# Performance work log

Measured on AMD Instinct MI355X. Metric: run time of the kernel, lower is better.

Reference implementation:

```python
import jax, jax.numpy as jnp
import numpy as np


def setup_inputs() -> dict:
    key = jax.random.key(0)
    ks = jax.random.split(key, 8)
    B, L, D, N, DM = 2, 2048, 2048, 8, 1024
    return {
        "x": jax.random.normal(ks[0], (B, L, D), jnp.float32),
        "A_log": jax.random.normal(ks[1], (D, N), jnp.float32),
        "x_proj_w": jax.random.normal(ks[2], (2 * N, D), jnp.float32) * (D ** -0.5),
        "x_proj_b": jax.random.normal(ks[3], (2 * N,), jnp.float32) * 0.02,
        "dt_proj_w": jax.random.normal(ks[4], (D, D), jnp.float32) * (D ** -0.5),
        "dt_proj_b": jax.random.normal(ks[5], (D,), jnp.float32) * 0.02,
        "out_proj_w": jax.random.normal(ks[6], (DM, D), jnp.float32) * (D ** -0.5),
        "out_proj_b": jax.random.normal(ks[7], (DM,), jnp.float32) * 0.02,
    }


def reference(x, A_log, x_proj_w, x_proj_b, dt_proj_w, dt_proj_b, out_proj_w, out_proj_b):
    # x: (B, L, D);  A_log: (D, N)
    A = -jnp.exp(A_log)                                   # (D, N), negative -> stable decay
    x_dbl = x @ x_proj_w.T + x_proj_b                     # (B, L, 2N): per-token B_t, C_t
    Bm, Cm = jnp.split(x_dbl, 2, axis=-1)                 # each (B, L, N)
    dt = jax.nn.softplus(x @ dt_proj_w.T + dt_proj_b)     # (B, L, D) selective timestep

    Bsz, L, D = x.shape
    N = A_log.shape[1]

    def step(h, inp):
        dt_t, B_t, C_t, x_t = inp                         # (B,D),(B,N),(B,N),(B,D)
        dA = jnp.exp(dt_t[..., None] * A)                 # (B, D, N)
        dB = dt_t[..., None] * B_t[:, None, :]            # (B, D, N)
        h = dA * h + dB * x_t[..., None]                  # (B, D, N)
        y = jnp.einsum("bdn,bn->bd", h, C_t)              # (B, D)
        return h, y

    h0 = jnp.zeros((Bsz, D, N), x.dtype)
    xs = (dt.transpose(1, 0, 2), Bm.transpose(1, 0, 2),
          Cm.transpose(1, 0, 2), x.transpose(1, 0, 2))
    _, ys = jax.lax.scan(step, h0, xs)                    # ys: (L, B, D)
    y = ys.transpose(1, 0, 2)                             # (B, L, D)
    return y @ out_proj_w.T + out_proj_b                  # (B, L, d_model)
```

## Files before the change

kernel.cpp:

```cpp
#include <hip/hip_runtime.h>
#include <hip/hip_bf16.h>

constexpr int Bsz = 2;
constexpr int L   = 2048;
constexpr int D   = 2048;
constexpr int Nst = 8;
constexpr int DM  = 1024;
constexpr int M   = Bsz * L;

constexpr int CH  = 64;
constexpr int T   = L / CH;
constexpr int BDN = Bsz * D * Nst;

typedef __bf16 bf16x8 __attribute__((ext_vector_type(8)));
typedef float f32x4 __attribute__((ext_vector_type(4)));

__global__ void cvt_f32_bf16(const float* __restrict__ in, __bf16* __restrict__ out, int n4) {
    int i = blockIdx.x * blockDim.x + threadIdx.x;
    if (i >= n4) return;
    float4 v = reinterpret_cast<const float4*>(in)[i];
    union { __bf16 b[4]; ushort4 u; } cv;
    cv.b[0] = (__bf16)v.x; cv.b[1] = (__bf16)v.y; cv.b[2] = (__bf16)v.z; cv.b[3] = (__bf16)v.w;
    reinterpret_cast<ushort4*>(out)[i] = cv.u;
}

__global__ __launch_bounds__(256) void xdbl_kernel(
    const float* __restrict__ x, const float* __restrict__ w,
    const float* __restrict__ bias, float* __restrict__ xdbl)
{
    const int lane = threadIdx.x & 63;
    const int row  = (blockIdx.x * blockDim.x + threadIdx.x) >> 6;
    if (row >= M) return;
    const float* xr = x + (size_t)row * D;
    float acc[16];
#pragma unroll
    for (int j = 0; j < 16; ++j) acc[j] = 0.f;
    for (int k = lane * 4; k < D; k += 64 * 4) {
        float4 xv = *reinterpret_cast<const float4*>(&xr[k]);
#pragma unroll
        for (int j = 0; j < 16; ++j) {
            float4 wv = *reinterpret_cast<const float4*>(&w[j * D + k]);
            acc[j] += xv.x * wv.x + xv.y * wv.y + xv.z * wv.z + xv.w * wv.w;
        }
    }
#pragma unroll
    for (int j = 0; j < 16; ++j) {
        float v = acc[j];
#pragma unroll
        for (int off = 32; off > 0; off >>= 1) v += __shfl_down(v, off, 64);
        if (lane == 0) xdbl[(size_t)row * 16 + j] = v + bias[j];
    }
}

__device__ inline void async16(__bf16* lds, const __bf16* g) {
    __builtin_amdgcn_global_load_lds(
        (const __attribute__((address_space(1))) void*)g,
        (__attribute__((address_space(3))) void*)lds, 16, 0, 0);
}

template <int MODE>
__global__ __launch_bounds__(256) void gemm_bt(
    const __bf16* __restrict__ A, const __bf16* __restrict__ Bw,
    const float* __restrict__ bias, float* __restrict__ C,
    int N, int K)
{
    constexpr int BM = 128, BN = 128, BK = 32;
    __shared__ __attribute__((aligned(16))) __bf16 lA[BM * BK];
    __shared__ __attribute__((aligned(16))) __bf16 lB[BN * BK];

    const int tid  = threadIdx.x;
    const int lane = tid & 63;
    const int wid  = tid >> 6;
    const int wm   = wid >> 1, wn = wid & 1;
    const int rowBase = blockIdx.y * BM;
    const int colBase = blockIdx.x * BN;
    const int lrow = lane & 15;
    const int kgrp = lane >> 4;

    f32x4 acc[4][4];
#pragma unroll
    for (int i = 0; i < 4; ++i)
#pragma unroll
        for (int j = 0; j < 4; ++j) acc[i][j] = f32x4{0.f, 0.f, 0.f, 0.f};

    const int sr = tid >> 2;
    const int sc = (tid & 3) * 8;
    const __bf16* gA0 = A  + (size_t)(rowBase + sr)      * K + sc;
    const __bf16* gA1 = A  + (size_t)(rowBase + sr + 64) * K + sc;
    const __bf16* gB0 = Bw + (size_t)(colBase + sr)      * K + sc;
    const __bf16* gB1 = Bw + (size_t)(colBase + sr + 64) * K + sc;
    __bf16* lA0p = &lA[tid * 8];
    __bf16* lA1p = &lA[2048 + tid * 8];
    __bf16* lB0p = &lB[tid * 8];
    __bf16* lB1p = &lB[2048 + tid * 8];

    for (int k0 = 0; k0 < K; k0 += BK) {
        async16(lA0p, gA0 + k0);
        async16(lA1p, gA1 + k0);
        async16(lB0p, gB0 + k0);
        async16(lB1p, gB1 + k0);
        __syncthreads();

        bf16x8 af[4], bfr[4];
#pragma unroll
        for (int m = 0; m < 4; ++m)
            af[m] = *reinterpret_cast<const bf16x8*>(&lA[(wm * 64 + m * 16 + lrow) * BK + kgrp * 8]);
#pragma unroll
        for (int n = 0; n < 4; ++n)
            bfr[n] = *reinterpret_cast<const bf16x8*>(&lB[(wn * 64 + n * 16 + lrow) * BK + kgrp * 8]);
#pragma unroll
        for (int m = 0; m < 4; ++m)
#pragma unroll
            for (int n = 0; n < 4; ++n)
                acc[m][n] = __builtin_amdgcn_mfma_f32_16x16x32_bf16(af[m], bfr[n], acc[m][n], 0, 0, 0);
        __syncthreads();
    }

#pragma unroll
    for (int m = 0; m < 4; ++m) {
        const int row = rowBase + wm * 64 + m * 16 + kgrp * 4;
#pragma unroll
        for (int n = 0; n < 4; ++n) {
            const int col = colBase + wn * 64 + n * 16 + lrow;
            const float bv = bias[col];
#pragma unroll
            for (int r = 0; r < 4; ++r) {
                float v = acc[m][n][r] + bv;
                if (MODE == 1) v = (v > 20.f) ? v : log1pf(expf(v));
                C[(size_t)(row + r) * N + col] = v;
            }
        }
    }
}

__global__ __launch_bounds__(64) void scan_p1(
    const float* __restrict__ dt, const float* __restrict__ x,
    const float* __restrict__ xdbl, const float* __restrict__ A_log,
    float* __restrict__ P, float* __restrict__ Hloc)
{
    const int tid = threadIdx.x;
    int blk = blockIdx.x;
    const int c  = blk % CH;  blk /= CH;
    const int dg = blk % (D / 64);
    const int b  = blk / (D / 64);
    const int d  = dg * 64 + tid;

    float A[Nst], h[Nst], p[Nst];
#pragma unroll
    for (int n = 0; n < Nst; ++n) {
        A[n] = -expf(A_log[(size_t)d * Nst + n]);
        h[n] = 0.f; p[n] = 1.f;
    }

    __shared__ __attribute__((aligned(16))) float sBC[T * 16];
    const float4* src = reinterpret_cast<const float4*>(xdbl + ((size_t)b * L + c * T) * 16);
#pragma unroll
    for (int i = tid; i < T * 4; i += 64)
        reinterpret_cast<float4*>(sBC)[i] = src[i];
    __syncthreads();

    const float* dt_p = dt + ((size_t)b * L + c * T) * D + d;
    const float* x_p  = x  + ((size_t)b * L + c * T) * D + d;
#pragma unroll 4
    for (int t2 = 0; t2 < T; ++t2) {
        const float dtv = dt_p[(size_t)t2 * D];
        const float xv  = x_p[(size_t)t2 * D];
        const float dtx = dtv * xv;
        const float* bc = &sBC[t2 * 16];
#pragma unroll
        for (int n = 0; n < Nst; ++n) {
            const float dA = __expf(dtv * A[n]);
            p[n] *= dA;
            h[n] = dA * h[n] + dtx * bc[n];
        }
    }
    const size_t base = ((size_t)c * Bsz * D + (size_t)b * D + d) * Nst;
#pragma unroll
    for (int n = 0; n < Nst; ++n) { P[base + n] = p[n]; Hloc[base + n] = h[n]; }
}

__global__ __launch_bounds__(256) void scan_p2(
    const float* __restrict__ P, const float* __restrict__ Hloc,
    float* __restrict__ Hstart)
{
    const int id = blockIdx.x * blockDim.x + threadIdx.x;
    if (id >= BDN) return;
    float h = 0.f;
    for (int c = 0; c < CH; ++c) {
        const size_t o = (size_t)c * BDN + id;
        Hstart[o] = h;
        h = P[o] * h + Hloc[o];
    }
}

__global__ __launch_bounds__(64) void scan_p3(
    const float* __restrict__ dt, const float* __restrict__ x,
    const float* __restrict__ xdbl, const float* __restrict__ A_log,
    const float* __restrict__ Hstart, __bf16* __restrict__ y_bf)
{
    const int tid = threadIdx.x;
    int blk = blockIdx.x;
    const int c  = blk % CH;  blk /= CH;
    const int dg = blk % (D / 64);
    const int b  = blk / (D / 64);
    const int d  = dg * 64 + tid;

    float A[Nst], h[Nst];
    const size_t hbase = ((size_t)c * Bsz * D + (size_t)b * D + d) * Nst;
#pragma unroll
    for (int n = 0; n < Nst; ++n) {
        A[n] = -expf(A_log[(size_t)d * Nst + n]);
        h[n] = Hstart[hbase + n];
    }

    __shared__ __attribute__((aligned(16))) float sBC[T * 16];
    const float4* src = reinterpret_cast<const float4*>(xdbl + ((size_t)b * L + c * T) * 16);
#pragma unroll
    for (int i = tid; i < T * 4; i += 64)
        reinterpret_cast<float4*>(sBC)[i] = src[i];
    __syncthreads();

    const float* dt_p = dt + ((size_t)b * L + c * T) * D + d;
    const float* x_p  = x  + ((size_t)b * L + c * T) * D + d;
    __bf16*      y_p  = y_bf + ((size_t)b * L + c * T) * D + d;
#pragma unroll 4
    for (int t2 = 0; t2 < T; ++t2) {
        const float dtv = dt_p[(size_t)t2 * D];
        const float xv  = x_p[(size_t)t2 * D];
        const float dtx = dtv * xv;
        const float* bc = &sBC[t2 * 16];
        float y = 0.f;
#pragma unroll
        for (int n = 0; n < Nst; ++n) {
            const float dA = __expf(dtv * A[n]);
            h[n] = dA * h[n] + dtx * bc[n];
            y = fmaf(h[n], bc[8 + n], y);
        }
        y_p[(size_t)t2 * D] = (__bf16)y;
    }
}

extern "C" void kernel_launch(void* const* d_in, const int* in_sizes, int n_in,
                              void* d_out, int out_size, void* d_ws, size_t ws_size,
                              hipStream_t stream) {
    const float* x     = (const float*)d_in[0];
    const float* A_log = (const float*)d_in[1];
    const float* xpw   = (const float*)d_in[2];
    const float* xpb   = (const float*)d_in[3];
    const float* dtw   = (const float*)d_in[4];
    const float* dtb   = (const float*)d_in[5];
    const float* ow    = (const float*)d_in[6];
    const float* ob    = (const float*)d_in[7];
    float* out = (float*)d_out;

    char* ws = (char*)d_ws;
    __bf16* x_bf   = (__bf16*)(ws);
    __bf16* dtw_bf = (__bf16*)(ws + 16777216);
    __bf16* ow_bf  = (__bf16*)(ws + 25165824);
    float*  xdbl   = (float* )(ws + 29360128);
    float*  dtbuf  = (float* )(ws + 29622272);
    __bf16* y_bf   = (__bf16*)(ws + 63176704);
    float*  P      = (float*)(ws);
    float*  Hloc   = (float*)(ws + 8388608);
    float*  Hstart = (float*)(ws + 16777216);

    cvt_f32_bf16<<<(M * D / 4 + 255) / 256, 256, 0, stream>>>(x, x_bf, M * D / 4);
    cvt_f32_bf16<<<(D * D / 4 + 255) / 256, 256, 0, stream>>>(dtw, dtw_bf, D * D / 4);
    cvt_f32_bf16<<<(DM * D / 4 + 255) / 256, 256, 0, stream>>>(ow, ow_bf, DM * D / 4);

    xdbl_kernel<<<M / 4, 256, 0, stream>>>(x, xpw, xpb, xdbl);

    gemm_bt<1><<<dim3(D / 128, M / 128), 256, 0, stream>>>(x_bf, dtw_bf, dtb, dtbuf, D, D);

    const int scan_blocks = Bsz * (D / 64) * CH;
    scan_p1<<<scan_blocks, 64, 0, stream>>>(dtbuf, x, xdbl, A_log, P, Hloc);
    scan_p2<<<(BDN + 255) / 256, 256, 0, stream>>>(P, Hloc, Hstart);
    scan_p3<<<scan_blocks, 64, 0, stream>>>(dtbuf, x, xdbl, A_log, Hstart, y_bf);

    gemm_bt<0><<<dim3(DM / 128, M / 128), 256, 0, stream>>>(y_bf, ow_bf, ob, out, DM, D);
}
```

Measured before the change: 225.9 us.

## Double-buffer GEMM with swizzled LDS and fuse x bf16 cast into xdbl

The bf16 GEMM moves to BK=64 with a two-stage double-buffered async global-to-LDS pipeline, XOR-swizzled LDS layout, hoisted bias loads, explicit waitcnt/barrier control and raised MFMA priority. This is meant to hide load latency and cut LDS bank conflicts. Separately, xdbl_kernel now caches the 16x2048 projection weight in LDS, processes 16 rows per block, and writes the bf16 copy of x itself, which removes a separate conversion pass over x. The 128KB LDS weight cache limits how many blocks fit per CU, and the hand-written vmcnt counts depend on the exact number of loads issued per stage.

New measurement: 185.8 us. 17.8% less time.

```diff
diff --git a/kernel.cpp b/kernel.cpp
--- a/kernel.cpp
+++ b/kernel.cpp
@@ -26,29 +26,43 @@
 
 __global__ __launch_bounds__(256) void xdbl_kernel(
     const float* __restrict__ x, const float* __restrict__ w,
-    const float* __restrict__ bias, float* __restrict__ xdbl)
-{
-    const int lane = threadIdx.x & 63;
-    const int row  = (blockIdx.x * blockDim.x + threadIdx.x) >> 6;
-    if (row >= M) return;
-    const float* xr = x + (size_t)row * D;
-    float acc[16];
-#pragma unroll
-    for (int j = 0; j < 16; ++j) acc[j] = 0.f;
-    for (int k = lane * 4; k < D; k += 64 * 4) {
-        float4 xv = *reinterpret_cast<const float4*>(&xr[k]);
+    const float* __restrict__ bias, float* __restrict__ xdbl,
+    __bf16* __restrict__ x_bf)
+{
+    __shared__ float sw[16 * 2048];
+    const int tid = threadIdx.x;
+    for (int i = tid; i < 16 * 2048 / 4; i += 256)
+        reinterpret_cast<float4*>(sw)[i] = reinterpret_cast<const float4*>(w)[i];
+    __syncthreads();
+
+    const int lane = tid & 63;
+    const int wrow = tid >> 6;
+    for (int rr = 0; rr < 4; ++rr) {
+        const int row = blockIdx.x * 16 + wrow * 4 + rr;
+        const float* xr = x + (size_t)row * D;
+        __bf16* xb = x_bf + (size_t)row * D;
+        float acc[16];
+#pragma unroll
+        for (int j = 0; j < 16; ++j) acc[j] = 0.f;
+        for (int k = lane * 4; k < D; k += 256) {
+            float4 xv = *reinterpret_cast<const float4*>(&xr[k]);
+            union { __bf16 b[4]; ushort4 u; } cv;
+            cv.b[0] = (__bf16)xv.x; cv.b[1] = (__bf16)xv.y;
+            cv.b[2] = (__bf16)xv.z; cv.b[3] = (__bf16)xv.w;
+            *reinterpret_cast<ushort4*>(&xb[k]) = cv.u;
+#pragma unroll
+            for (int j = 0; j < 16; ++j) {
+                float4 wv = *reinterpret_cast<const float4*>(&sw[j * D + k]);
+                acc[j] += xv.x * wv.x + xv.y * wv.y + xv.z * wv.z + xv.w * wv.w;
+            }
+        }
 #pragma unroll
         for (int j = 0; j < 16; ++j) {
-            float4 wv = *reinterpret_cast<const float4*>(&w[j * D + k]);
-            acc[j] += xv.x * wv.x + xv.y * wv.y + xv.z * wv.z + xv.w * wv.w;
-        }
-    }
-#pragma unroll
-    for (int j = 0; j < 16; ++j) {
-        float v = acc[j];
-#pragma unroll
-        for (int off = 32; off > 0; off >>= 1) v += __shfl_down(v, off, 64);
-        if (lane == 0) xdbl[(size_t)row * 16 + j] = v + bias[j];
+            float v = acc[j];
+#pragma unroll
+            for (int off = 32; off > 0; off >>= 1) v += __shfl_down(v, off, 64);
+            if (lane == 0) xdbl[(size_t)row * 16 + j] = v + bias[j];
+        }
     }
 }
 
@@ -59,14 +73,14 @@
 }
 
 template <int MODE>
-__global__ __launch_bounds__(256) void gemm_bt(
+__global__ __launch_bounds__(256, 2) void gemm_bt(
     const __bf16* __restrict__ A, const __bf16* __restrict__ Bw,
     const float* __restrict__ bias, float* __restrict__ C,
     int N, int K)
 {
-    constexpr int BM = 128, BN = 128, BK = 32;
-    __shared__ __attribute__((aligned(16))) __bf16 lA[BM * BK];
-    __shared__ __attribute__((aligned(16))) __bf16 lB[BN * BK];
+    constexpr int BM = 128, BN = 128, BK = 64;
+    const int NT = K / BK;
+    __shared__ __attribute__((aligned(16))) __bf16 lds[2][2][BM * BK];
 
     const int tid  = threadIdx.x;
     const int lane = tid & 63;
@@ -77,43 +91,78 @@
     const int lrow = lane & 15;
     const int kgrp = lane >> 4;
 
+    float bv[4];
+#pragma unroll
+    for (int n = 0; n < 4; ++n) bv[n] = bias[colBase + wn * 64 + n * 16 + lrow];
+    asm volatile("s_waitcnt vmcnt(0)" ::: "memory");
+
+    const int trow = tid >> 3;
+    const int scol = ((tid & 7) ^ (trow & 7)) * 8;
+    const __bf16* gA[4]; const __bf16* gB[4];
+#pragma unroll
+    for (int ro = 0; ro < 4; ++ro) {
+        gA[ro] = A  + (size_t)(rowBase + ro * 32 + trow) * K + scol;
+        gB[ro] = Bw + (size_t)(colBase + ro * 32 + trow) * K + scol;
+    }
+
     f32x4 acc[4][4];
 #pragma unroll
     for (int i = 0; i < 4; ++i)
 #pragma unroll
         for (int j = 0; j < 4; ++j) acc[i][j] = f32x4{0.f, 0.f, 0.f, 0.f};
 
-    const int sr = tid >> 2;
-    const int sc = (tid & 3) * 8;
-    const __bf16* gA0 = A  + (size_t)(rowBase + sr)      * K + sc;
-    const __bf16* gA1 = A  + (size_t)(rowBase + sr + 64) * K + sc;
-    const __bf16* gB0 = Bw + (size_t)(colBase + sr)      * K + sc;
-    const __bf16* gB1 = Bw + (size_t)(colBase + sr + 64) * K + sc;
-    __bf16* lA0p = &lA[tid * 8];
-    __bf16* lA1p = &lA[2048 + tid * 8];
-    __bf16* lB0p = &lB[tid * 8];
-    __bf16* lB1p = &lB[2048 + tid * 8];
-
-    for (int k0 = 0; k0 < K; k0 += BK) {
-        async16(lA0p, gA0 + k0);
-        async16(lA1p, gA1 + k0);
-        async16(lB0p, gB0 + k0);
-        async16(lB1p, gB1 + k0);
-        __syncthreads();
-
-        bf16x8 af[4], bfr[4];
-#pragma unroll
-        for (int m = 0; m < 4; ++m)
-            af[m] = *reinterpret_cast<const bf16x8*>(&lA[(wm * 64 + m * 16 + lrow) * BK + kgrp * 8]);
-#pragma unroll
-        for (int n = 0; n < 4; ++n)
-            bfr[n] = *reinterpret_cast<const bf16x8*>(&lB[(wn * 64 + n * 16 + lrow) * BK + kgrp * 8]);
-#pragma unroll
-        for (int m = 0; m < 4; ++m)
-#pragma unroll
-            for (int n = 0; n < 4; ++n)
-                acc[m][n] = __builtin_amdgcn_mfma_f32_16x16x32_bf16(af[m], bfr[n], acc[m][n], 0, 0, 0);
-        __syncthreads();
+    auto stage = [&](int kt, int bsel) {
+        const int k0 = kt * BK;
+#pragma unroll
+        for (int ro = 0; ro < 4; ++ro) {
+            async16(&lds[bsel][0][ro * 2048 + tid * 8], gA[ro] + k0);
+            async16(&lds[bsel][1][ro * 2048 + tid * 8], gB[ro] + k0);
+        }
+    };
+
+    stage(0, 0);
+    stage(1, 1);
+
+    for (int t = 0; t < NT; ++t) {
+        if (t == NT - 1) asm volatile("s_waitcnt vmcnt(0)" ::: "memory");
+        else             asm volatile("s_waitcnt vmcnt(8)" ::: "memory");
+        __builtin_amdgcn_s_barrier();
+
+        const int cur = t & 1;
+        bf16x8 af[4][2], bfr[4][2];
+#pragma unroll
+        for (int m = 0; m < 4; ++m) {
+            const int row = wm * 64 + m * 16 + lrow;
+#pragma unroll
+            for (int kk = 0; kk < 2; ++kk) {
+                const int slot = (kk * 4 + kgrp) ^ (lrow & 7);
+                af[m][kk] = *reinterpret_cast<const bf16x8*>(&lds[cur][0][row * 64 + slot * 8]);
+            }
+        }
+#pragma unroll
+        for (int n = 0; n < 4; ++n) {
+            const int row = wn * 64 + n * 16 + lrow;
+#pragma unroll
+            for (int kk = 0; kk < 2; ++kk) {
+                const int slot = (kk * 4 + kgrp) ^ (lrow & 7);
+                bfr[n][kk] = *reinterpret_cast<const bf16x8*>(&lds[cur][1][row * 64 + slot * 8]);
+            }
+        }
+        asm volatile("s_waitcnt lgkmcnt(0)" ::: "memory");
+        __builtin_amdgcn_sched_barrier(0);
+        __builtin_amdgcn_s_barrier();
+
+        if (t + 2 < NT) stage(t + 2, cur);
+
+        __builtin_amdgcn_s_setprio(1);
+#pragma unroll
+        for (int kk = 0; kk < 2; ++kk)
+#pragma unroll
+            for (int m = 0; m < 4; ++m)
+#pragma unroll
+                for (int n = 0; n < 4; ++n)
+                    acc[m][n] = __builtin_amdgcn_mfma_f32_16x16x32_bf16(af[m][kk], bfr[n][kk], acc[m][n], 0, 0, 0);
+        __builtin_amdgcn_s_setprio(0);
     }
 
 #pragma unroll
@@ -122,10 +171,9 @@
 #pragma unroll
         for (int n = 0; n < 4; ++n) {
             const int col = colBase + wn * 64 + n * 16 + lrow;
-            const float bv = bias[col];
 #pragma unroll
             for (int r = 0; r < 4; ++r) {
-                float v = acc[m][n][r] + bv;
+                float v = acc[m][n][r] + bv[n];
                 if (MODE == 1) v = (v > 20.f) ? v : log1pf(expf(v));
                 C[(size_t)(row + r) * N + col] = v;
             }
@@ -264,11 +312,10 @@
     float*  Hloc   = (float*)(ws + 8388608);
     float*  Hstart = (float*)(ws + 16777216);
 
-    cvt_f32_bf16<<<(M * D / 4 + 255) / 256, 256, 0, stream>>>(x, x_bf, M * D / 4);
     cvt_f32_bf16<<<(D * D / 4 + 255) / 256, 256, 0, stream>>>(dtw, dtw_bf, D * D / 4);
     cvt_f32_bf16<<<(DM * D / 4 + 255) / 256, 256, 0, stream>>>(ow, ow_bf, DM * D / 4);
 
-    xdbl_kernel<<<M / 4, 256, 0, stream>>>(x, xpw, xpb, xdbl);
+    xdbl_kernel<<<M / 16, 256, 0, stream>>>(x, xpw, xpb, xdbl, x_bf);
 
     gemm_bt<1><<<dim3(D / 128, M / 128), 256, 0, stream>>>(x_bf, dtw_bf, dtb, dtbuf, D, D);
 
```
